# Optimization experiments

Hardware: AMD Instinct MI355X
Metric: run time of the kernel (lower is better)

Reference implementation:

```python
import jax, jax.numpy as jnp
import numpy as np

ALPHA = 0.2  # LeakyReLU negative slope
NEG_BIG = -9e15


def setup_inputs() -> dict:
    key = jax.random.key(0)
    k1, k2, k3, k4 = jax.random.split(key, 4)
    N, F_IN, F_OUT = 8192, 256, 128
    h = jax.random.normal(k1, (N, F_IN), dtype=jnp.float32)
    adj = jax.random.randint(k2, (N, N), 0, 2, dtype=jnp.int32)
    # xavier_uniform with gain=1.414
    def xavier(k, shape, gain=1.414):
        fan_in, fan_out = shape[0], shape[1]
        bound = gain * np.sqrt(6.0 / (fan_in + fan_out))
        return jax.random.uniform(k, shape, jnp.float32, -bound, bound)
    W = xavier(k3, (F_IN, F_OUT))
    a = xavier(k4, (2 * F_OUT, 1))
    return {"h": h, "adj": adj, "W": W, "a": a}


def reference(h, adj, W, a):
    # Wh: [N, F_out]
    Wh = h @ W
    F_out = W.shape[1]
    a1 = a[:F_out, 0]   # attends to source (row) node
    a2 = a[F_out:, 0]   # attends to target (col) node
    # Additive decomposition of concat([Wh_i, Wh_j]) @ a:
    # e[i, j] = leaky_relu(Wh_i . a1 + Wh_j . a2)
    f1 = Wh @ a1  # [N]
    f2 = Wh @ a2  # [N]
    e = jax.nn.leaky_relu(f1[:, None] + f2[None, :], negative_slope=ALPHA)  # [N, N]
    scores = jnp.where(adj > 0, e, jnp.float32(NEG_BIG))
    attention = jax.nn.softmax(scores, axis=1)
    # dropout is identity in eval mode (training=False)
    h_prime = attention @ Wh  # [N, F_out]
    return h_prime
```

## Files before the change

### kernel.cpp

```cpp
#include <hip/hip_runtime.h>


#define N_NODES 8192
#define F_IN 256
#define F_OUT 128
#define NJT 32
#define JTW 256
#define NCH 8
#define LDS_STRIDE 264

typedef _Float16 half8 __attribute__((ext_vector_type(8)));
typedef float floatx4 __attribute__((ext_vector_type(4)));
typedef float f32x4 __attribute__((ext_vector_type(4)));
typedef int intx4 __attribute__((ext_vector_type(4)));

__device__ __align__(16) _Float16 g_WhT[(size_t)F_OUT * N_NODES];
__device__ __align__(16) float g_f1[N_NODES];
__device__ __align__(16) float g_f2[N_NODES];
__device__ __align__(16) float g_part[NJT][N_NODES * F_OUT];
__device__ __align__(16) float g_spart[NJT][N_NODES];
__device__ __align__(16) unsigned char g_bits[(size_t)N_NODES * (N_NODES / 8)];

__global__ __launch_bounds__(256, 2) void prep_kernel(
    const int* __restrict__ adj, const float* __restrict__ h,
    const float* __restrict__ W, const float* __restrict__ a) {
  const int t = threadIdx.x;
  const int bid = blockIdx.x;

  if (bid % 3 != 0) {
    const int pid = bid - (bid + 2) / 3;
    const int wave = t >> 6;
    const int lane = t & 63;
    const int row0 = pid * 8 + wave * 2;
#pragma unroll 1
    for (int rr = 0; rr < 2; ++rr) {
      const int r = row0 + rr;
      const int* rowp = adj + (size_t)r * N_NODES;
#pragma unroll 4
      for (int p = 0; p < 16; ++p) {
        const int j0 = p * 512 + lane * 8;
        const intx4 v0 = __builtin_nontemporal_load((const intx4*)(rowp + j0));
        const intx4 v1 = __builtin_nontemporal_load((const intx4*)(rowp + j0 + 4));
        unsigned int byte = 0;
        byte |= (v0.x != 0) ? 1u : 0u;
        byte |= (v0.y != 0) ? 2u : 0u;
        byte |= (v0.z != 0) ? 4u : 0u;
        byte |= (v0.w != 0) ? 8u : 0u;
        byte |= (v1.x != 0) ? 16u : 0u;
        byte |= (v1.y != 0) ? 32u : 0u;
        byte |= (v1.z != 0) ? 64u : 0u;
        byte |= (v1.w != 0) ? 128u : 0u;
        const int b = p * 64 + lane;
        g_bits[(size_t)r * 1024 + (b & 3) * 256 + (b >> 2)] = (unsigned char)byte;
      }
    }
    return;
  }

  __shared__ float hT[F_IN][20];
  __shared__ float fs[2][2][8][2];
  const int i0 = (bid / 3) * 16;
  {
    const int row = t >> 4;
    const int fu = t & 15;
#pragma unroll
    for (int r = 0; r < 4; ++r) {
      const int ku = r * 16 + fu;
      const f32x4 v = __builtin_nontemporal_load(
          (const f32x4*)(h + (size_t)(i0 + row) * F_IN + ku * 4));
      hT[ku * 4 + 0][row] = v.x; hT[ku * 4 + 1][row] = v.y;
      hT[ku * 4 + 2][row] = v.z; hT[ku * 4 + 3][row] = v.w;
    }
  }
  __syncthreads();
  const int c = t & 127;
  const int rg = t >> 7;
  float acc[8];
#pragma unroll
  for (int r = 0; r < 8; ++r) acc[r] = 0.f;
#pragma unroll 8
  for (int k = 0; k < F_IN; ++k) {
    const float wv = W[k * F_OUT + c];
    const float4 x0 = *(const float4*)(&hT[k][rg * 8]);
    const float4 x1 = *(const float4*)(&hT[k][rg * 8 + 4]);
    acc[0] = fmaf(x0.x, wv, acc[0]); acc[1] = fmaf(x0.y, wv, acc[1]);
    acc[2] = fmaf(x0.z, wv, acc[2]); acc[3] = fmaf(x0.w, wv, acc[3]);
    acc[4] = fmaf(x1.x, wv, acc[4]); acc[5] = fmaf(x1.y, wv, acc[5]);
    acc[6] = fmaf(x1.z, wv, acc[6]); acc[7] = fmaf(x1.w, wv, acc[7]);
  }
  union { _Float16 hh[8]; uint4 u4; } pk;
#pragma unroll
  for (int r = 0; r < 8; ++r) pk.hh[r] = (_Float16)acc[r];
  *(uint4*)(g_WhT + (size_t)c * N_NODES + i0 + rg * 8) = pk.u4;

  const float a1c = a[c];
  const float a2c = a[F_OUT + c];
  float p1[8], p2[8];
#pragma unroll
  for (int r = 0; r < 8; ++r) { p1[r] = acc[r] * a1c; p2[r] = acc[r] * a2c; }
#pragma unroll
  for (int o = 32; o > 0; o >>= 1)
#pragma unroll
    for (int r = 0; r < 8; ++r) {
      p1[r] += __shfl_down(p1[r], o, 64);
      p2[r] += __shfl_down(p2[r], o, 64);
    }
  const int wv = t >> 6;
  const int lane = t & 63;
  if (lane == 0) {
#pragma unroll
    for (int r = 0; r < 8; ++r) {
      fs[wv >> 1][wv & 1][r][0] = p1[r];
      fs[wv >> 1][wv & 1][r][1] = p2[r];
    }
  }
  __syncthreads();
  if (t < 16) {
    const int rg2 = t >> 3, r2 = t & 7;
    g_f1[i0 + rg2 * 8 + r2] = fs[rg2][0][r2][0] + fs[rg2][1][r2][0];
    g_f2[i0 + rg2 * 8 + r2] = fs[rg2][0][r2][1] + fs[rg2][1][r2][1];
  }
}

__device__ __forceinline__ float score_b(unsigned int bit, float f2v, float f1r) {
  float s = f1r + f2v;
  s = fmaxf(s, 0.2f * s);
  float arg = bit ? fmaf(s, 1.44269504088896f, -16.0f) : -1.0e5f;
  return __builtin_amdgcn_exp2f(arg);
}

__global__ __launch_bounds__(512, 2) void gat_attn_kernel() {
  const int t = threadIdx.x;
  const int wave = t >> 6;
  const int lane = t & 63;
  const int mrow = lane & 15;
  const int quad = lane >> 4;
  const int bid = blockIdx.x;
  const int jt = bid >> 5;
  const int ig = bid & 31;
  const int rowb = ig * 256 + wave * 32;

  __shared__ _Float16 ldsWhT[F_OUT * LDS_STRIDE];
  __shared__ float ldsF2[JTW];

  const int r0 = rowb + mrow, r1 = rowb + 16 + mrow;
  const uint2 AB0 = *(const uint2*)(g_bits + (size_t)r0 * 1024 + quad * 256 + jt * 8);
  const uint2 AB1 = *(const uint2*)(g_bits + (size_t)r1 * 1024 + quad * 256 + jt * 8);
  const float f1r0 = g_f1[r0];
  const float f1r1 = g_f1[r1];

  int rm[4], cm[4];
  {
    half8 a1f, b1f, a2f, b2f;
#pragma unroll
    for (int e = 0; e < 8; ++e) {
      a1f[e] = (_Float16)0; b1f[e] = (_Float16)0;
      a2f[e] = (_Float16)0; b2f[e] = (_Float16)0;
    }
    if (quad == 0) {
      a1f[0] = (_Float16)mrow; b1f[0] = (_Float16)1;
      a2f[0] = (_Float16)1;    b2f[0] = (_Float16)mrow;
    }
    floatx4 d1 = (floatx4)0.f, d2 = (floatx4)0.f;
    d1 = __builtin_amdgcn_mfma_f32_16x16x32_f16(a1f, b1f, d1, 0, 0, 0);
    d2 = __builtin_amdgcn_mfma_f32_16x16x32_f16(a2f, b2f, d2, 0, 0, 0);
#pragma unroll
    for (int r = 0; r < 4; ++r) { rm[r] = (int)d1[r]; cm[r] = (int)d2[r]; }
  }

#pragma unroll
  for (int it = 0; it < 8; ++it) {
    const int idx = it * 512 + t;
    const int row = idx >> 5, cu = idx & 31;
    *(half8*)&ldsWhT[row * LDS_STRIDE + cu * 8] =
        *(const half8*)(g_WhT + (size_t)row * N_NODES + jt * JTW + cu * 8);
  }
  if (t < 64) *(float4*)&ldsF2[t * 4] = *(const float4*)(g_f2 + jt * JTW + t * 4);
  __syncthreads();

  half8 ones;
#pragma unroll
  for (int e = 0; e < 8; ++e) ones[e] = (_Float16)1;

  floatx4 acc[2][8];
  floatx4 asum[2];
#pragma unroll
  for (int tl = 0; tl < 2; ++tl) {
    asum[tl] = (floatx4)0.f;
#pragma unroll
    for (int ct = 0; ct < 8; ++ct) acc[tl][ct] = (floatx4)0.f;
  }

#pragma unroll
  for (int ch = 0; ch < NCH; ++ch) {
    const int kb = ch * 32 + quad * 8;

    half8 bfr[8];
#pragma unroll
    for (int ct = 0; ct < 8; ++ct)
      bfr[ct] = *(const half8*)&ldsWhT[(ct * 16 + mrow) * LDS_STRIDE + kb];

    const float4 F0 = *(const float4*)&ldsF2[kb];
    const float4 F1 = *(const float4*)&ldsF2[kb + 4];

    const unsigned int b0 = ((ch & 4) ? AB0.y : AB0.x) >> ((ch & 3) * 8);
    const unsigned int b1 = ((ch & 4) ? AB1.y : AB1.x) >> ((ch & 3) * 8);

    half8 af0, af1;
    af0[0] = (_Float16)score_b(b0 & 1u,   F0.x, f1r0);
    af0[1] = (_Float16)score_b(b0 & 2u,   F0.y, f1r0);
    af0[2] = (_Float16)score_b(b0 & 4u,   F0.z, f1r0);
    af0[3] = (_Float16)score_b(b0 & 8u,   F0.w, f1r0);
    af0[4] = (_Float16)score_b(b0 & 16u,  F1.x, f1r0);
    af0[5] = (_Float16)score_b(b0 & 32u,  F1.y, f1r0);
    af0[6] = (_Float16)score_b(b0 & 64u,  F1.z, f1r0);
    af0[7] = (_Float16)score_b(b0 & 128u, F1.w, f1r0);
    af1[0] = (_Float16)score_b(b1 & 1u,   F0.x, f1r1);
    af1[1] = (_Float16)score_b(b1 & 2u,   F0.y, f1r1);
    af1[2] = (_Float16)score_b(b1 & 4u,   F0.z, f1r1);
    af1[3] = (_Float16)score_b(b1 & 8u,   F0.w, f1r1);
    af1[4] = (_Float16)score_b(b1 & 16u,  F1.x, f1r1);
    af1[5] = (_Float16)score_b(b1 & 32u,  F1.y, f1r1);
    af1[6] = (_Float16)score_b(b1 & 64u,  F1.z, f1r1);
    af1[7] = (_Float16)score_b(b1 & 128u, F1.w, f1r1);

#pragma unroll
    for (int ct = 0; ct < 8; ++ct) {
      acc[0][ct] = __builtin_amdgcn_mfma_f32_16x16x32_f16(af0, bfr[ct], acc[0][ct], 0, 0, 0);
      acc[1][ct] = __builtin_amdgcn_mfma_f32_16x16x32_f16(af1, bfr[ct], acc[1][ct], 0, 0, 0);
    }
    asum[0] = __builtin_amdgcn_mfma_f32_16x16x32_f16(af0, ones, asum[0], 0, 0, 0);
    asum[1] = __builtin_amdgcn_mfma_f32_16x16x32_f16(af1, ones, asum[1], 0, 0, 0);
  }

  float* pslice = g_part[jt];
#pragma unroll
  for (int tl = 0; tl < 2; ++tl)
#pragma unroll
    for (int ct = 0; ct < 8; ++ct)
#pragma unroll
      for (int r = 0; r < 4; ++r)
        pslice[(size_t)(rowb + tl * 16 + rm[r]) * F_OUT + ct * 16 + cm[r]] =
            acc[tl][ct][r];
  if (mrow == 0) {
#pragma unroll
    for (int tl = 0; tl < 2; ++tl)
#pragma unroll
      for (int r = 0; r < 4; ++r)
        g_spart[jt][rowb + tl * 16 + rm[r]] = asum[tl][r];
  }
}

__global__ __launch_bounds__(256) void comb_kernel(float* __restrict__ out) {
  const int u = blockIdx.x * 256 + threadIdx.x;
  const int row = u >> 5;
  float s = 0.f;
  f32x4 v = (f32x4)0.f;
#pragma unroll
  for (int q = 0; q < NJT; ++q) {
    s += g_spart[q][row];
    v += *(((const f32x4*)g_part[q]) + u);
  }
  __builtin_nontemporal_store(v * (1.0f / s), ((f32x4*)out) + u);
}

extern "C" void kernel_launch(void* const* d_in, const int* in_sizes, int n_in,
                              void* d_out, int out_size, void* d_ws, size_t ws_size,
                              hipStream_t stream) {
  const float* h = (const float*)d_in[0];
  const int* adj = (const int*)d_in[1];
  const float* W = (const float*)d_in[2];
  const float* a = (const float*)d_in[3];
  float* out = (float*)d_out;
  (void)d_ws; (void)ws_size;

  prep_kernel<<<dim3(1536), dim3(256), 0, stream>>>(adj, h, W, a);
  gat_attn_kernel<<<dim3(NJT * 32), dim3(512), 0, stream>>>();
  comb_kernel<<<dim3(N_NODES * F_OUT / 4 / 256), dim3(256), 0, stream>>>(out);
}
```

Baseline: 432.0 us.

## Halve row tile per wave and loop two column tiles per block to shrink partials

Each block now covers 128 rows (16 per wave) and processes two consecutive 256-column tiles in a loop, writing to 16 partial slices instead of 32. This halves the partial-sum buffer traffic written by the attention kernel and read by the combine kernel, and raises the occupancy target to four blocks per CU. In exchange, each WhT tile loaded into LDS is reused by fewer rows, so LDS fill traffic per row doubles, and an extra barrier sits between tiles. The output-coordinate mapping now uses the fixed MFMA layout instead of one derived at runtime by a probe MFMA.

```diff
diff --git a/kernel.cpp b/kernel.cpp
--- a/kernel.cpp
+++ b/kernel.cpp
@@ -7,6 +7,7 @@
 #define NJT 32
 #define JTW 256
 #define NCH 8
+#define NSL 16
 #define LDS_STRIDE 264
 
 typedef _Float16 half8 __attribute__((ext_vector_type(8)));
@@ -17,8 +18,8 @@
 __device__ __align__(16) _Float16 g_WhT[(size_t)F_OUT * N_NODES];
 __device__ __align__(16) float g_f1[N_NODES];
 __device__ __align__(16) float g_f2[N_NODES];
-__device__ __align__(16) float g_part[NJT][N_NODES * F_OUT];
-__device__ __align__(16) float g_spart[NJT][N_NODES];
+__device__ __align__(16) float g_part[NSL][N_NODES * F_OUT];
+__device__ __align__(16) float g_spart[NSL][N_NODES];
 __device__ __align__(16) unsigned char g_bits[(size_t)N_NODES * (N_NODES / 8)];
 
 __global__ __launch_bounds__(256, 2) void prep_kernel(
@@ -129,125 +130,91 @@
   return __builtin_amdgcn_exp2f(arg);
 }
 
-__global__ __launch_bounds__(512, 2) void gat_attn_kernel() {
+__global__ __launch_bounds__(512, 4) void gat_attn_kernel() {
   const int t = threadIdx.x;
   const int wave = t >> 6;
   const int lane = t & 63;
   const int mrow = lane & 15;
   const int quad = lane >> 4;
   const int bid = blockIdx.x;
-  const int jt = bid >> 5;
-  const int ig = bid & 31;
-  const int rowb = ig * 256 + wave * 32;
+  const int jtg = bid >> 6;
+  const int ig = bid & 63;
+  const int rowb = ig * 128 + wave * 16;
 
   __shared__ _Float16 ldsWhT[F_OUT * LDS_STRIDE];
   __shared__ float ldsF2[JTW];
 
-  const int r0 = rowb + mrow, r1 = rowb + 16 + mrow;
-  const uint2 AB0 = *(const uint2*)(g_bits + (size_t)r0 * 1024 + quad * 256 + jt * 8);
-  const uint2 AB1 = *(const uint2*)(g_bits + (size_t)r1 * 1024 + quad * 256 + jt * 8);
+  const int r0 = rowb + mrow;
+  const uint4 AB = *(const uint4*)(g_bits + (size_t)r0 * 1024 + quad * 256 + jtg * 16);
   const float f1r0 = g_f1[r0];
-  const float f1r1 = g_f1[r1];
-
-  int rm[4], cm[4];
-  {
-    half8 a1f, b1f, a2f, b2f;
-#pragma unroll
-    for (int e = 0; e < 8; ++e) {
-      a1f[e] = (_Float16)0; b1f[e] = (_Float16)0;
-      a2f[e] = (_Float16)0; b2f[e] = (_Float16)0;
-    }
-    if (quad == 0) {
-      a1f[0] = (_Float16)mrow; b1f[0] = (_Float16)1;
-      a2f[0] = (_Float16)1;    b2f[0] = (_Float16)mrow;
-    }
-    floatx4 d1 = (floatx4)0.f, d2 = (floatx4)0.f;
-    d1 = __builtin_amdgcn_mfma_f32_16x16x32_f16(a1f, b1f, d1, 0, 0, 0);
-    d2 = __builtin_amdgcn_mfma_f32_16x16x32_f16(a2f, b2f, d2, 0, 0, 0);
-#pragma unroll
-    for (int r = 0; r < 4; ++r) { rm[r] = (int)d1[r]; cm[r] = (int)d2[r]; }
-  }
-
-#pragma unroll
-  for (int it = 0; it < 8; ++it) {
-    const int idx = it * 512 + t;
-    const int row = idx >> 5, cu = idx & 31;
-    *(half8*)&ldsWhT[row * LDS_STRIDE + cu * 8] =
-        *(const half8*)(g_WhT + (size_t)row * N_NODES + jt * JTW + cu * 8);
-  }
-  if (t < 64) *(float4*)&ldsF2[t * 4] = *(const float4*)(g_f2 + jt * JTW + t * 4);
-  __syncthreads();
 
   half8 ones;
 #pragma unroll
   for (int e = 0; e < 8; ++e) ones[e] = (_Float16)1;
 
-  floatx4 acc[2][8];
-  floatx4 asum[2];
-#pragma unroll
-  for (int tl = 0; tl < 2; ++tl) {
-    asum[tl] = (floatx4)0.f;
-#pragma unroll
-    for (int ct = 0; ct < 8; ++ct) acc[tl][ct] = (floatx4)0.f;
-  }
-
-#pragma unroll
-  for (int ch = 0; ch < NCH; ++ch) {
-    const int kb = ch * 32 + quad * 8;
-
-    half8 bfr[8];
-#pragma unroll
-    for (int ct = 0; ct < 8; ++ct)
-      bfr[ct] = *(const half8*)&ldsWhT[(ct * 16 + mrow) * LDS_STRIDE + kb];
-
-    const float4 F0 = *(const float4*)&ldsF2[kb];
-    const float4 F1 = *(const float4*)&ldsF2[kb + 4];
-
-    const unsigned int b0 = ((ch & 4) ? AB0.y : AB0.x) >> ((ch & 3) * 8);
-    const unsigned int b1 = ((ch & 4) ? AB1.y : AB1.x) >> ((ch & 3) * 8);
-
-    half8 af0, af1;
-    af0[0] = (_Float16)score_b(b0 & 1u,   F0.x, f1r0);
-    af0[1] = (_Float16)score_b(b0 & 2u,   F0.y, f1r0);
-    af0[2] = (_Float16)score_b(b0 & 4u,   F0.z, f1r0);
-    af0[3] = (_Float16)score_b(b0 & 8u,   F0.w, f1r0);
-    af0[4] = (_Float16)score_b(b0 & 16u,  F1.x, f1r0);
-    af0[5] = (_Float16)score_b(b0 & 32u,  F1.y, f1r0);
-    af0[6] = (_Float16)score_b(b0 & 64u,  F1.z, f1r0);
-    af0[7] = (_Float16)score_b(b0 & 128u, F1.w, f1r0);
-    af1[0] = (_Float16)score_b(b1 & 1u,   F0.x, f1r1);
-    af1[1] = (_Float16)score_b(b1 & 2u,   F0.y, f1r1);
-    af1[2] = (_Float16)score_b(b1 & 4u,   F0.z, f1r1);
-    af1[3] = (_Float16)score_b(b1 & 8u,   F0.w, f1r1);
-    af1[4] = (_Float16)score_b(b1 & 16u,  F1.x, f1r1);
-    af1[5] = (_Float16)score_b(b1 & 32u,  F1.y, f1r1);
-    af1[6] = (_Float16)score_b(b1 & 64u,  F1.z, f1r1);
-    af1[7] = (_Float16)score_b(b1 & 128u, F1.w, f1r1);
-
-#pragma unroll
-    for (int ct = 0; ct < 8; ++ct) {
-      acc[0][ct] = __builtin_amdgcn_mfma_f32_16x16x32_f16(af0, bfr[ct], acc[0][ct], 0, 0, 0);
-      acc[1][ct] = __builtin_amdgcn_mfma_f32_16x16x32_f16(af1, bfr[ct], acc[1][ct], 0, 0, 0);
-    }
-    asum[0] = __builtin_amdgcn_mfma_f32_16x16x32_f16(af0, ones, asum[0], 0, 0, 0);
-    asum[1] = __builtin_amdgcn_mfma_f32_16x16x32_f16(af1, ones, asum[1], 0, 0, 0);
-  }
-
-  float* pslice = g_part[jt];
-#pragma unroll
-  for (int tl = 0; tl < 2; ++tl)
-#pragma unroll
-    for (int ct = 0; ct < 8; ++ct)
-#pragma unroll
-      for (int r = 0; r < 4; ++r)
-        pslice[(size_t)(rowb + tl * 16 + rm[r]) * F_OUT + ct * 16 + cm[r]] =
-            acc[tl][ct][r];
+  floatx4 acc[8];
+  floatx4 asum = (floatx4)0.f;
+#pragma unroll
+  for (int ct = 0; ct < 8; ++ct) acc[ct] = (floatx4)0.f;
+
+#pragma unroll
+  for (int tp = 0; tp < 2; ++tp) {
+    const int jt = jtg * 2 + tp;
+    if (tp) __syncthreads();
+
+#pragma unroll
+    for (int it = 0; it < 8; ++it) {
+      const int idx = it * 512 + t;
+      const int row = idx >> 5, cu = idx & 31;
+      *(half8*)&ldsWhT[row * LDS_STRIDE + cu * 8] =
+          *(const half8*)(g_WhT + (size_t)row * N_NODES + jt * JTW + cu * 8);
+    }
+    if (t < 64) *(float4*)&ldsF2[t * 4] = *(const float4*)(g_f2 + jt * JTW + t * 4);
+    __syncthreads();
+
+#pragma unroll
+    for (int ch = 0; ch < NCH; ++ch) {
+      const int kb = ch * 32 + quad * 8;
+
+      half8 bfr[8];
+#pragma unroll
+      for (int ct = 0; ct < 8; ++ct)
+        bfr[ct] = *(const half8*)&ldsWhT[(ct * 16 + mrow) * LDS_STRIDE + kb];
+
+      const float4 F0 = *(const float4*)&ldsF2[kb];
+      const float4 F1 = *(const float4*)&ldsF2[kb + 4];
+
+      const unsigned int dw = tp ? ((ch & 4) ? AB.w : AB.z)
+                                 : ((ch & 4) ? AB.y : AB.x);
+      const unsigned int b0 = dw >> ((ch & 3) * 8);
+
+      half8 af0;
+      af0[0] = (_Float16)score_b(b0 & 1u,   F0.x, f1r0);
+      af0[1] = (_Float16)score_b(b0 & 2u,   F0.y, f1r0);
+      af0[2] = (_Float16)score_b(b0 & 4u,   F0.z, f1r0);
+      af0[3] = (_Float16)score_b(b0 & 8u,   F0.w, f1r0);
+      af0[4] = (_Float16)score_b(b0 & 16u,  F1.x, f1r0);
+      af0[5] = (_Float16)score_b(b0 & 32u,  F1.y, f1r0);
+      af0[6] = (_Float16)score_b(b0 & 64u,  F1.z, f1r0);
+      af0[7] = (_Float16)score_b(b0 & 128u, F1.w, f1r0);
+
+#pragma unroll
+      for (int ct = 0; ct < 8; ++ct)
+        acc[ct] = __builtin_amdgcn_mfma_f32_16x16x32_f16(af0, bfr[ct], acc[ct], 0, 0, 0);
+      asum = __builtin_amdgcn_mfma_f32_16x16x32_f16(af0, ones, asum, 0, 0, 0);
+    }
+  }
+
+  float* pslice = g_part[jtg];
+#pragma unroll
+  for (int ct = 0; ct < 8; ++ct)
+#pragma unroll
+    for (int r = 0; r < 4; ++r)
+      pslice[(size_t)(rowb + quad * 4 + r) * F_OUT + ct * 16 + mrow] = acc[ct][r];
   if (mrow == 0) {
 #pragma unroll
-    for (int tl = 0; tl < 2; ++tl)
-#pragma unroll
-      for (int r = 0; r < 4; ++r)
-        g_spart[jt][rowb + tl * 16 + rm[r]] = asum[tl][r];
+    for (int r = 0; r < 4; ++r)
+      g_spart[jtg][rowb + quad * 4 + r] = asum[r];
   }
 }
 
@@ -257,7 +224,7 @@
   float s = 0.f;
   f32x4 v = (f32x4)0.f;
 #pragma unroll
-  for (int q = 0; q < NJT; ++q) {
+  for (int q = 0; q < NSL; ++q) {
     s += g_spart[q][row];
     v += *(((const f32x4*)g_part[q]) + u);
   }
@@ -275,6 +242,6 @@
   (void)d_ws; (void)ws_size;
 
   prep_kernel<<<dim3(1536), dim3(256), 0, stream>>>(adj, h, W, a);
-  gat_attn_kernel<<<dim3(NJT * 32), dim3(512), 0, stream>>>();
+  gat_attn_kernel<<<dim3(64 * NSL), dim3(512), 0, stream>>>();
   comb_kernel<<<dim3(N_NODES * F_OUT / 4 / 256), dim3(256), 0, stream>>>(out);
 }
```

Result: faster. 411.2 us (-4.8%).
